# Kernel optimization log

Hardware: AMD Instinct MI355X
Metric: run time of the kernel (lower is better)

Reference implementation:

```python
import jax, jax.numpy as jnp
import numpy as np

D_MODEL = 2048
N_HEADS = 16
HEAD_DIM = D_MODEL // N_HEADS


def setup_inputs() -> dict:
    key = jax.random.key(0)
    k_x, k_wqkv, k_bqkv, k_wo, k_bo = jax.random.split(key, 5)
    s = 1.0 / np.sqrt(D_MODEL)
    return {
        "x": jax.random.normal(k_x, (2, 2048, D_MODEL), dtype=jnp.float32),
        "w_qkv": jax.random.uniform(k_wqkv, (D_MODEL, 3 * D_MODEL), jnp.float32, -s, s),
        "b_qkv": jax.random.uniform(k_bqkv, (3 * D_MODEL,), jnp.float32, -s, s),
        "w_out": jax.random.uniform(k_wo, (D_MODEL, D_MODEL), jnp.float32, -s, s),
        "b_out": jax.random.uniform(k_bo, (D_MODEL,), jnp.float32, -s, s),
    }


def reference(x, w_qkv, b_qkv, w_out, b_out):
    b, l, d = x.shape
    h, e = N_HEADS, HEAD_DIM
    qkv = x @ w_qkv + b_qkv                       # [b, l, 3d]
    q, k, v = jnp.split(qkv, 3, axis=-1)
    # split heads: [b, l, d] -> [b, l, h, e]
    q = q.reshape(b, l, h, e)
    k = k.reshape(b, l, h, e)
    v = v.reshape(b, l, h, e)
    scale = 1.0 / np.sqrt(e).astype(np.float32)
    scores = jnp.einsum("bqhe,bkhe->bhqk", q, k) * scale  # [b, h, l, l]
    attn = jax.nn.softmax(scores, axis=-1)                 # non-causal (module hardcodes is_causal=False)
    out = jnp.einsum("bhqk,bkhe->bqhe", attn, v)           # [b, l, h, e]
    out = out.reshape(b, l, d)                             # merge heads
    return out @ w_out + b_out
```

## Files before the change

### kernel.cpp

```cpp
#include <hip/hip_runtime.h>

typedef __attribute__((ext_vector_type(8))) short bf16x8;
typedef __attribute__((ext_vector_type(4))) float f32x4;
typedef __attribute__((ext_vector_type(16))) float f32x16;
typedef __attribute__((ext_vector_type(4))) int int4v;
typedef __attribute__((ext_vector_type(4))) unsigned short us4;

#define LOG2E 1.4426950408889634f

__device__ __forceinline__ unsigned short f2b(float f){
  unsigned u = __builtin_bit_cast(unsigned, f);
  u = (u + 0x7fffu + ((u >> 16) & 1u)) >> 16;
  return (unsigned short)u;
}
__device__ __forceinline__ unsigned short f2bf(float f){
  unsigned u = __builtin_bit_cast(unsigned, f);
  return (unsigned short)((u + 0x8000u) >> 16);
}

__device__ __forceinline__ f32x4 mfma16(bf16x8 a, bf16x8 b, f32x4 c){
  return __builtin_amdgcn_mfma_f32_16x16x32_bf16(a, b, c, 0, 0, 0);
}
__device__ __forceinline__ f32x16 mfma32(bf16x8 a, bf16x8 b, f32x16 c){
  return __builtin_amdgcn_mfma_f32_32x32x16_bf16(a, b, c, 0, 0, 0);
}

typedef const __attribute__((address_space(1))) void* gas_t;
typedef __attribute__((address_space(3))) void* las_t;
__device__ __forceinline__ void glds16(const void* g, void* l){
  __builtin_amdgcn_global_load_lds((gas_t)g, (las_t)l, 16, 0, 0);
}

__global__ __launch_bounds__(256) void cast_bf16_kernel(const float4* __restrict__ in,
                                                        us4* __restrict__ out, int n4){
  int i = blockIdx.x * 256 + threadIdx.x;
  int stride = gridDim.x * 256;
  for (; i < n4; i += stride){
    float4 v = in[i];
    us4 o; o.x = f2b(v.x); o.y = f2b(v.y); o.z = f2b(v.z); o.w = f2b(v.w);
    out[i] = o;
  }
}

__global__ __launch_bounds__(256) void transpose_cast_kernel(const float* __restrict__ in,
                                                             unsigned short* __restrict__ out,
                                                             int R, int C){
  __shared__ float tile[64][65];
  const int tid = threadIdx.x;
  const int c0 = blockIdx.x * 64, r0 = blockIdx.y * 64;
#pragma unroll
  for (int p = 0; p < 4; p++){
    int idx = p * 1024 + tid * 4;
    int rr = idx >> 6, cc = idx & 63;
    float4 v = *(const float4*)(in + (size_t)(r0 + rr) * C + (c0 + cc));
    tile[rr][cc+0] = v.x; tile[rr][cc+1] = v.y; tile[rr][cc+2] = v.z; tile[rr][cc+3] = v.w;
  }
  __syncthreads();
#pragma unroll
  for (int p = 0; p < 4; p++){
    int idx = p * 1024 + tid * 4;
    int crow = idx >> 6, rcol = idx & 63;
    us4 o;
    o.x = f2b(tile[rcol+0][crow]); o.y = f2b(tile[rcol+1][crow]);
    o.z = f2b(tile[rcol+2][crow]); o.w = f2b(tile[rcol+3][crow]);
    *(us4*)(out + (size_t)(c0 + crow) * R + (r0 + rcol)) = o;
  }
}

template<int MODE>
__global__ __launch_bounds__(256, 2) void gemm_kernel(
    const unsigned short* __restrict__ A,
    const unsigned short* __restrict__ BT,
    const float* __restrict__ bias,
    unsigned short* __restrict__ qb,
    unsigned short* __restrict__ kb,
    unsigned short* __restrict__ vtb,
    float* __restrict__ outp)
{
  constexpr int K = 2048;
  constexpr int NT = K / 64;
  __shared__ short lA[2][128 * 64];
  __shared__ short lB[2][128 * 64];
  const int tid = threadIdx.x, lane = tid & 63, wid = tid >> 6;
  const int l16 = lane & 15, lhi = lane >> 4;
  const int wr = wid >> 1, wc = wid & 1;
  const int bm = blockIdx.x, bn = blockIdx.y;

  const char* Abase = (const char*)(A + (size_t)bm * 128 * K);
  const char* Bbase = (const char*)(BT + (size_t)bn * 128 * K);

  const char* agp[4]; const char* bgp[4];
  int dst[4];
#pragma unroll
  for (int i = 0; i < 4; i++){
    int c = wid * 4 + i;
    int row = c * 8 + (lane >> 3);
    int col = ((lane & 7) * 16) ^ ((lane >> 3) << 4);
    agp[i] = Abase + (size_t)row * (K * 2) + col;
    bgp[i] = Bbase + (size_t)row * (K * 2) + col;
    dst[i] = c * 1024;
  }

  auto stage = [&](int kt, int buf){
    char* bA = (char*)lA[buf]; char* bB = (char*)lB[buf];
#pragma unroll
    for (int i = 0; i < 4; i++){
      glds16(agp[i] + kt * 128, bA + dst[i]);
      glds16(bgp[i] + kt * 128, bB + dst[i]);
    }
  };

  f32x4 acc[4][4];
  f32x4 z = {0.f, 0.f, 0.f, 0.f};
#pragma unroll
  for (int i = 0; i < 4; i++)
#pragma unroll
    for (int j = 0; j < 4; j++) acc[i][j] = z;

  stage(0, 0);
  __syncthreads();
  int cur = 0;
  for (int kt = 0; kt < NT; ++kt){
    if (kt + 1 < NT) stage(kt + 1, cur ^ 1);
#pragma unroll
    for (int kk = 0; kk < 2; kk++){
      bf16x8 af[4], bfr[4];
#pragma unroll
      for (int mf = 0; mf < 4; mf++){
        int row = wr * 64 + mf * 16 + l16;
        int byte = (row * 128 + kk * 64 + lhi * 16) ^ ((row & 7) << 4);
        af[mf] = *(const bf16x8*)((const char*)lA[cur] + byte);
      }
#pragma unroll
      for (int nf = 0; nf < 4; nf++){
        int row = wc * 64 + nf * 16 + l16;
        int byte = (row * 128 + kk * 64 + lhi * 16) ^ ((row & 7) << 4);
        bfr[nf] = *(const bf16x8*)((const char*)lB[cur] + byte);
      }
      __builtin_amdgcn_s_setprio(1);
#pragma unroll
      for (int mf = 0; mf < 4; mf++)
#pragma unroll
        for (int nf = 0; nf < 4; nf++)
          acc[mf][nf] = mfma16(af[mf], bfr[nf], acc[mf][nf]);
      __builtin_amdgcn_s_setprio(0);
    }
    __syncthreads();
    cur ^= 1;
  }

  const int row0 = bm * 128 + wr * 64;
  const int col0 = bn * 128 + wc * 64;
  if (MODE == 0){
#pragma unroll
    for (int nf = 0; nf < 4; nf++){
      int colb = col0 + nf * 16;
      float bv = bias[colb + l16];
      int which = colb >> 11;
      int h = (colb >> 7) & 15;
      int e = (colb & 127) + l16;
#pragma unroll
      for (int mf = 0; mf < 4; mf++){
#pragma unroll
        for (int r = 0; r < 4; r++){
          int row = row0 + mf * 16 + lhi * 4 + r;
          int b = row >> 11, t = row & 2047;
          float v = acc[mf][nf][r] + bv;
          size_t bh = (size_t)(b * 16 + h);
          if (which == 0)      qb[(bh * 2048 + t) * 128 + e] = f2b(v * 0.08838834764831845f);
          else if (which == 1) kb[(bh * 2048 + t) * 128 + e] = f2b(v);
          else                 vtb[(bh * 128 + e) * 2048 + t] = f2b(v);
        }
      }
    }
  } else {
#pragma unroll
    for (int nf = 0; nf < 4; nf++){
      int col = col0 + nf * 16 + l16;
      float bv = bias[col];
#pragma unroll
      for (int mf = 0; mf < 4; mf++){
#pragma unroll
        for (int r = 0; r < 4; r++){
          int row = row0 + mf * 16 + lhi * 4 + r;
          outp[(size_t)row * 2048 + col] = acc[mf][nf][r] + bv;
        }
      }
    }
  }
}

__global__ __launch_bounds__(256, 2) void attn_kernel(
    const unsigned short* __restrict__ q_buf,
    const unsigned short* __restrict__ k_buf,
    const unsigned short* __restrict__ vt_buf,
    unsigned short* __restrict__ attn_out)
{
  constexpr int L = 2048, NT = L / 64;
  __shared__ short lK[2][64 * 128];
  __shared__ short lVT[2][128 * 64];
  const int tid = threadIdx.x, lane = tid & 63, wid = tid >> 6;
  const int l31 = lane & 31, lhi2 = lane >> 5;

  const int d = blockIdx.y * 16 + blockIdx.x;
  const int bh = (d & 7) + 8 * ((d >> 3) & 3);
  const int qi = d >> 5;
  const int qbase = qi * 128;

  const unsigned short* qp = q_buf + (size_t)bh * L * 128;
  const char* kp2 = (const char*)(k_buf + (size_t)bh * L * 128);
  const char* vp2 = (const char*)(vt_buf + (size_t)bh * 128 * L);

  bf16x8 qf[8];
  {
    const unsigned short* qr = qp + (size_t)(qbase + wid * 32 + l31) * 128 + lhi2 * 8;
#pragma unroll
    for (int kk = 0; kk < 8; kk++)
      qf[kk] = *(const bf16x8*)(qr + kk * 16);
  }

  const char* kgp[4]; const char* vgp[4];
  int kdst[4], vdst[4];
#pragma unroll
  for (int i = 0; i < 4; i++){
    int c = wid * 4 + i;
    { int row = c * 4 + (lane >> 4);
      int col = ((lane & 15) * 16) ^ ((row & 7) << 4);
      kgp[i] = kp2 + row * 256 + col;
      kdst[i] = c * 1024; }
    { int e = c * 8 + (lane >> 3);
      int col = ((lane & 7) * 16) ^ ((e & 7) << 4);
      vgp[i] = vp2 + (size_t)e * 4096 + col;
      vdst[i] = c * 1024; }
  }

  auto stage = [&](int kt, int buf){
    char* bK = (char*)lK[buf]; char* bV = (char*)lVT[buf];
#pragma unroll
    for (int i = 0; i < 4; i++){
      glds16(kgp[i] + kt * 16384, bK + kdst[i]);
      glds16(vgp[i] + (size_t)kt * 128, bV + vdst[i]);
    }
  };

  f32x16 oacc[4];
#pragma unroll
  for (int nf = 0; nf < 4; nf++)
#pragma unroll
    for (int j = 0; j < 16; j++) oacc[nf][j] = 0.f;
  float m = -1e30f, ml2 = 0.f, lsum = 0.f;

  stage(0, 0);
  __syncthreads();
  int cur = 0;
  for (int kt = 0; kt < NT; ++kt){
    if (kt + 1 < NT) stage(kt + 1, cur ^ 1);
    const char* cK = (const char*)lK[cur];
    const char* cV = (const char*)lVT[cur];

    f32x16 sf[2];
#pragma unroll
    for (int mf = 0; mf < 2; mf++)
#pragma unroll
      for (int j = 0; j < 16; j++) sf[mf][j] = 0.f;
    __builtin_amdgcn_s_setprio(1);
#pragma unroll
    for (int kk = 0; kk < 8; kk++){
#pragma unroll
      for (int mf = 0; mf < 2; mf++){
        int byte = ((l31 * 256 + kk * 32 + lhi2 * 16) ^ ((l31 & 7) << 4)) + mf * 8192;
        bf16x8 kf = *(const bf16x8*)(cK + byte);
        sf[mf] = mfma32(kf, qf[kk], sf[mf]);
      }
    }
    __builtin_amdgcn_s_setprio(0);

    float tm = sf[0][0];
#pragma unroll
    for (int mf = 0; mf < 2; mf++)
#pragma unroll
      for (int j = 0; j < 16; j++) tm = fmaxf(tm, sf[mf][j]);
    tm = fmaxf(tm, __shfl_xor(tm, 32, 64));

    if (!__all(tm <= m + 8.0f)){
      float mn = fmaxf(m, tm);
      float alpha = __builtin_exp2f((m - mn) * LOG2E);
      m = mn; ml2 = mn * LOG2E;
      lsum *= alpha;
#pragma unroll
      for (int reg = 0; reg < 16; reg++){
        int row = (reg & 3) + 8 * (reg >> 2) + 4 * lhi2;
        float ar = __shfl(alpha, row | (lane & 32), 64);
#pragma unroll
        for (int nf = 0; nf < 4; nf++) oacc[nf][reg] *= ar;
      }
    }

    float pex[2][16];
    float rs = 0.f;
#pragma unroll
    for (int mf = 0; mf < 2; mf++)
#pragma unroll
      for (int j = 0; j < 16; j++){
        float p = __builtin_exp2f(__builtin_fmaf(sf[mf][j], LOG2E, -ml2));
        pex[mf][j] = p; rs += p;
      }
    rs += __shfl_xor(rs, 32, 64);
    lsum += rs;

    unsigned W[2][4][2];
#pragma unroll
    for (int mf = 0; mf < 2; mf++)
#pragma unroll
      for (int g = 0; g < 4; g++)
#pragma unroll
        for (int h = 0; h < 2; h++)
          W[mf][g][h] = (unsigned)f2bf(pex[mf][g * 4 + 2 * h]) |
                        ((unsigned)f2bf(pex[mf][g * 4 + 2 * h + 1]) << 16);

    __builtin_amdgcn_s_setprio(1);
#pragma unroll
    for (int kk2 = 0; kk2 < 4; kk2++){
      const int mfp = kk2 >> 1, gA = 2 * (kk2 & 1), gB = gA + 1;
      unsigned A0 = W[mfp][gA][0], A1 = W[mfp][gA][1];
      unsigned B0 = W[mfp][gB][0], B1 = W[mfp][gB][1];
      unsigned own0 = lhi2 ? B0 : A0, own1 = lhi2 ? B1 : A1;
      unsigned snd0 = lhi2 ? A0 : B0, snd1 = lhi2 ? A1 : B1;
      unsigned rcv0 = (unsigned)__shfl_xor((int)snd0, 32, 64);
      unsigned rcv1 = (unsigned)__shfl_xor((int)snd1, 32, 64);
      int4v pw;
      pw.x = (int)(lhi2 ? rcv0 : own0);
      pw.y = (int)(lhi2 ? rcv1 : own1);
      pw.z = (int)(lhi2 ? own0 : rcv0);
      pw.w = (int)(lhi2 ? own1 : rcv1);
      bf16x8 pa = __builtin_bit_cast(bf16x8, pw);
#pragma unroll
      for (int nf = 0; nf < 4; nf++){
        int byte = ((l31 * 128 + kk2 * 32 + lhi2 * 16) ^ ((l31 & 7) << 4)) + nf * 4096;
        bf16x8 vb = *(const bf16x8*)(cV + byte);
        oacc[nf] = mfma32(pa, vb, oacc[nf]);
      }
    }
    __builtin_amdgcn_s_setprio(0);

    __syncthreads();
    cur ^= 1;
  }

  const int b = bh >> 4, h = bh & 15;
  float rl = 1.0f / lsum;
#pragma unroll
  for (int reg = 0; reg < 16; reg++){
    int row = (reg & 3) + 8 * (reg >> 2) + 4 * lhi2;
    float rr = __shfl(rl, row | (lane & 32), 64);
    size_t base = ((size_t)(b * L + qbase + wid * 32 + row)) * 2048 + h * 128 + l31;
#pragma unroll
    for (int nf = 0; nf < 4; nf++)
      attn_out[base + nf * 32] = f2b(oacc[nf][reg] * rr);
  }
}

extern "C" void kernel_launch(void* const* d_in, const int* in_sizes, int n_in,
                              void* d_out, int out_size, void* d_ws, size_t ws_size,
                              hipStream_t stream) {
  const float* x     = (const float*)d_in[0];
  const float* w_qkv = (const float*)d_in[1];
  const float* b_qkv = (const float*)d_in[2];
  const float* w_out = (const float*)d_in[3];
  const float* b_out = (const float*)d_in[4];
  float* out = (float*)d_out;

  unsigned short* ws = (unsigned short*)d_ws;
  unsigned short* xb    = ws;
  unsigned short* wqkvT = xb    + (size_t)4096 * 2048;
  unsigned short* woutT = wqkvT + (size_t)6144 * 2048;
  unsigned short* qb    = woutT + (size_t)2048 * 2048;
  unsigned short* kb    = qb    + (size_t)2 * 16 * 2048 * 128;
  unsigned short* vtb   = kb    + (size_t)2 * 16 * 2048 * 128;
  unsigned short* attnb = vtb   + (size_t)2 * 16 * 2048 * 128;

  cast_bf16_kernel<<<2048, 256, 0, stream>>>((const float4*)x, (us4*)xb, (4096 * 2048) / 4);
  transpose_cast_kernel<<<dim3(96, 32), 256, 0, stream>>>(w_qkv, wqkvT, 2048, 6144);
  transpose_cast_kernel<<<dim3(32, 32), 256, 0, stream>>>(w_out, woutT, 2048, 2048);
  gemm_kernel<0><<<dim3(32, 48), 256, 0, stream>>>(xb, wqkvT, b_qkv, qb, kb, vtb, nullptr);
  attn_kernel<<<dim3(16, 32), 256, 0, stream>>>(qb, kb, vtb, attnb);
  gemm_kernel<1><<<dim3(32, 16), 256, 0, stream>>>(attnb, woutT, b_out, nullptr, nullptr, nullptr, out);
}
```

Before: 280.0 us.

## Widen GEMM tiles to 128x256 with 512 threads and explicit vmcnt pipelining

The GEMM kernel now uses 512-thread blocks, eight waves each owning a 64x64 output tile, so every block covers a 128x256 output tile. The B tile buffer doubles in size, and the grid halves along N for both the QKV and output projections. The main loop now issues the next two stages ahead, uses explicit s_waitcnt vmcnt plus raw s_barrier instead of __syncthreads, and refills a buffer right after its last read. This is meant to raise A-tile reuse and overlap global loads with MFMA work, at the cost of more LDS per block, one block per CU, and fewer blocks for the output GEMM (256).

```diff
diff --git a/kernel.cpp b/kernel.cpp
--- a/kernel.cpp
+++ b/kernel.cpp
@@ -68,7 +68,7 @@
 }
 
 template<int MODE>
-__global__ __launch_bounds__(256, 2) void gemm_kernel(
+__global__ __launch_bounds__(512, 1) void gemm_kernel(
     const unsigned short* __restrict__ A,
     const unsigned short* __restrict__ BT,
     const float* __restrict__ bias,
@@ -80,34 +80,37 @@
   constexpr int K = 2048;
   constexpr int NT = K / 64;
   __shared__ short lA[2][128 * 64];
-  __shared__ short lB[2][128 * 64];
+  __shared__ short lB[2][256 * 64];
   const int tid = threadIdx.x, lane = tid & 63, wid = tid >> 6;
   const int l16 = lane & 15, lhi = lane >> 4;
-  const int wr = wid >> 1, wc = wid & 1;
+  const int wm = wid >> 2, wn = wid & 3;
   const int bm = blockIdx.x, bn = blockIdx.y;
 
   const char* Abase = (const char*)(A + (size_t)bm * 128 * K);
-  const char* Bbase = (const char*)(BT + (size_t)bn * 128 * K);
-
-  const char* agp[4]; const char* bgp[4];
-  int dst[4];
-#pragma unroll
-  for (int i = 0; i < 4; i++){
-    int c = wid * 4 + i;
-    int row = c * 8 + (lane >> 3);
-    int col = ((lane & 7) * 16) ^ ((lane >> 3) << 4);
-    agp[i] = Abase + (size_t)row * (K * 2) + col;
-    bgp[i] = Bbase + (size_t)row * (K * 2) + col;
-    dst[i] = c * 1024;
+  const char* Bbase = (const char*)(BT + (size_t)bn * 256 * K);
+
+  const int scol = ((lane & 7) * 16) ^ ((lane >> 3) << 4);
+  const char* agp[2]; const char* bgp[4];
+  int adst[2], bdst[4];
+#pragma unroll
+  for (int j = 0; j < 2; j++){
+    int row = j * 64 + wid * 8 + (lane >> 3);
+    agp[j] = Abase + (size_t)row * (K * 2) + scol;
+    adst[j] = (j * 64 + wid * 8) * 128;
+  }
+#pragma unroll
+  for (int j = 0; j < 4; j++){
+    int row = j * 64 + wid * 8 + (lane >> 3);
+    bgp[j] = Bbase + (size_t)row * (K * 2) + scol;
+    bdst[j] = (j * 64 + wid * 8) * 128;
   }
 
   auto stage = [&](int kt, int buf){
     char* bA = (char*)lA[buf]; char* bB = (char*)lB[buf];
 #pragma unroll
-    for (int i = 0; i < 4; i++){
-      glds16(agp[i] + kt * 128, bA + dst[i]);
-      glds16(bgp[i] + kt * 128, bB + dst[i]);
-    }
+    for (int j = 0; j < 2; j++) glds16(agp[j] + kt * 128, bA + adst[j]);
+#pragma unroll
+    for (int j = 0; j < 4; j++) glds16(bgp[j] + kt * 128, bB + bdst[j]);
   };
 
   f32x4 acc[4][4];
@@ -117,25 +120,30 @@
 #pragma unroll
     for (int j = 0; j < 4; j++) acc[i][j] = z;
 
-  stage(0, 0);
-  __syncthreads();
-  int cur = 0;
-  for (int kt = 0; kt < NT; ++kt){
-    if (kt + 1 < NT) stage(kt + 1, cur ^ 1);
+  stage(0, 0); stage(1, 1);
+
+  for (int t = 0; t < NT; ++t){
+    const int c = t & 1;
+    if (t < NT - 1) asm volatile("s_waitcnt vmcnt(6)" ::: "memory");
+    else            asm volatile("s_waitcnt vmcnt(0)" ::: "memory");
+    __builtin_amdgcn_sched_barrier(0);
+    __builtin_amdgcn_s_barrier();
+    __builtin_amdgcn_sched_barrier(0);
+
 #pragma unroll
     for (int kk = 0; kk < 2; kk++){
       bf16x8 af[4], bfr[4];
 #pragma unroll
       for (int mf = 0; mf < 4; mf++){
-        int row = wr * 64 + mf * 16 + l16;
+        int row = wm * 64 + mf * 16 + l16;
         int byte = (row * 128 + kk * 64 + lhi * 16) ^ ((row & 7) << 4);
-        af[mf] = *(const bf16x8*)((const char*)lA[cur] + byte);
+        af[mf] = *(const bf16x8*)((const char*)lA[c] + byte);
       }
 #pragma unroll
       for (int nf = 0; nf < 4; nf++){
-        int row = wc * 64 + nf * 16 + l16;
+        int row = wn * 64 + nf * 16 + l16;
         int byte = (row * 128 + kk * 64 + lhi * 16) ^ ((row & 7) << 4);
-        bfr[nf] = *(const bf16x8*)((const char*)lB[cur] + byte);
+        bfr[nf] = *(const bf16x8*)((const char*)lB[c] + byte);
       }
       __builtin_amdgcn_s_setprio(1);
 #pragma unroll
@@ -145,12 +153,16 @@
           acc[mf][nf] = mfma16(af[mf], bfr[nf], acc[mf][nf]);
       __builtin_amdgcn_s_setprio(0);
     }
-    __syncthreads();
-    cur ^= 1;
-  }
-
-  const int row0 = bm * 128 + wr * 64;
-  const int col0 = bn * 128 + wc * 64;
+
+    asm volatile("s_waitcnt lgkmcnt(0)" ::: "memory");
+    __builtin_amdgcn_sched_barrier(0);
+    __builtin_amdgcn_s_barrier();
+    __builtin_amdgcn_sched_barrier(0);
+    if (t + 2 < NT) stage(t + 2, c);
+  }
+
+  const int row0 = bm * 128 + wm * 64;
+  const int col0 = bn * 256 + wn * 64;
   if (MODE == 0){
 #pragma unroll
     for (int nf = 0; nf < 4; nf++){
@@ -382,7 +394,7 @@
   cast_bf16_kernel<<<2048, 256, 0, stream>>>((const float4*)x, (us4*)xb, (4096 * 2048) / 4);
   transpose_cast_kernel<<<dim3(96, 32), 256, 0, stream>>>(w_qkv, wqkvT, 2048, 6144);
   transpose_cast_kernel<<<dim3(32, 32), 256, 0, stream>>>(w_out, woutT, 2048, 2048);
-  gemm_kernel<0><<<dim3(32, 48), 256, 0, stream>>>(xb, wqkvT, b_qkv, qb, kb, vtb, nullptr);
+  gemm_kernel<0><<<dim3(32, 24), 512, 0, stream>>>(xb, wqkvT, b_qkv, qb, kb, vtb, nullptr);
   attn_kernel<<<dim3(16, 32), 256, 0, stream>>>(qb, kb, vtb, attnb);
-  gemm_kernel<1><<<dim3(32, 16), 256, 0, stream>>>(attnb, woutT, b_out, nullptr, nullptr, nullptr, out);
-}
+  gemm_kernel<1><<<dim3(32, 8), 512, 0, stream>>>(attnb, woutT, b_out, nullptr, nullptr, nullptr, out);
+}
```

After: 306.0 us. 9.3% more time.

## Use 256x256 eight-wave GEMM with quadrant-phased pipelining for QKV projection

Applied to the files above, without the earlier changes.

Replaces the QKV projection GEMM with a new 512-thread kernel that computes 256x256 output tiles. Each K step is split into four quadrant phases that interleave LDS fragment reads, async global-to-LDS staging of the next tile half, barriers and MFMA bursts at raised priority. Both GEMMs now launch as 1D grids remapped so that groups of blocks sharing the same A rows run together, to improve L2 reuse. The larger tile raises arithmetic intensity but uses 128KB of LDS and allows one block per CU. It also depends on precise vmcnt bookkeeping, which is fragile.

```diff
diff --git a/kernel.cpp b/kernel.cpp
--- a/kernel.cpp
+++ b/kernel.cpp
@@ -30,6 +30,10 @@
 __device__ __forceinline__ void glds16(const void* g, void* l){
   __builtin_amdgcn_global_load_lds((gas_t)g, (las_t)l, 16, 0, 0);
 }
+
+#define VMW(N) asm volatile("s_waitcnt vmcnt(" #N ")" ::: "memory")
+#define BARX() do{ __builtin_amdgcn_sched_barrier(0); __builtin_amdgcn_s_barrier(); \
+                   __builtin_amdgcn_sched_barrier(0); }while(0)
 
 __global__ __launch_bounds__(256) void cast_bf16_kernel(const float4* __restrict__ in,
                                                         us4* __restrict__ out, int n4){
@@ -64,6 +68,121 @@
     o.x = f2b(tile[rcol+0][crow]); o.y = f2b(tile[rcol+1][crow]);
     o.z = f2b(tile[rcol+2][crow]); o.w = f2b(tile[rcol+3][crow]);
     *(us4*)(out + (size_t)(c0 + crow) * R + (r0 + rcol)) = o;
+  }
+}
+
+__global__ __launch_bounds__(512, 1) void gemm8_kernel(
+    const unsigned short* __restrict__ A,
+    const unsigned short* __restrict__ BT,
+    const float* __restrict__ bias,
+    unsigned short* __restrict__ qb,
+    unsigned short* __restrict__ kb,
+    unsigned short* __restrict__ vtb)
+{
+  constexpr int K = 2048;
+  constexpr int NT = K / 64;
+  __shared__ short lds[2][4][128 * 64];
+  const int tid = threadIdx.x, lane = tid & 63, wid = tid >> 6;
+  const int l16 = lane & 15, lhi = lane >> 4;
+  const int wm = wid >> 2, wn = wid & 3;
+
+  const int id = blockIdx.x;
+  const int logical = (id & 7) * 48 + (id >> 3);
+  const int bm = logical & 15, bn = logical >> 4;
+
+  const char* Ab = (const char*)(A + (size_t)bm * 256 * K);
+  const char* Bb = (const char*)(BT + (size_t)bn * 256 * K);
+
+  const int scol = ((lane & 7) * 16) ^ ((lane >> 3) << 4);
+  const char* gsrc[4][2];
+  int gdst[2];
+#pragma unroll
+  for (int j = 0; j < 2; j++){
+    int r = j * 64 + wid * 8 + (lane >> 3);
+    gdst[j] = (j * 64 + wid * 8) * 128;
+    gsrc[0][j] = Ab + (size_t)(r      ) * (K * 2) + scol;
+    gsrc[1][j] = Ab + (size_t)(r + 128) * (K * 2) + scol;
+    gsrc[2][j] = Bb + (size_t)(r      ) * (K * 2) + scol;
+    gsrc[3][j] = Bb + (size_t)(r + 128) * (K * 2) + scol;
+  }
+  auto stageH = [&](int kt, int buf, int h){
+    char* dstb = (char*)lds[buf][h];
+#pragma unroll
+    for (int j = 0; j < 2; j++) glds16(gsrc[h][j] + (size_t)kt * 128, dstb + gdst[j]);
+  };
+
+  f32x4 acc[8][4];
+  f32x4 z = {0.f, 0.f, 0.f, 0.f};
+#pragma unroll
+  for (int i = 0; i < 8; i++)
+#pragma unroll
+    for (int j = 0; j < 4; j++) acc[i][j] = z;
+
+#define PHASE(MQ, NQ, SH)                                                        \
+  {                                                                              \
+    bf16x8 af[4][2], bfr[2][2];                                                  \
+    const char* aH = (const char*)lds[cur][MQ];                                  \
+    const char* bH = (const char*)lds[cur][2 + NQ];                              \
+    _Pragma("unroll")                                                            \
+    for (int mf2 = 0; mf2 < 4; mf2++){                                           \
+      int r = wm * 64 + mf2 * 16 + l16;                                          \
+      _Pragma("unroll")                                                          \
+      for (int kk = 0; kk < 2; kk++)                                             \
+        af[mf2][kk] = *(const bf16x8*)(aH + ((r * 128 + kk * 64 + lhi * 16) ^ ((r & 7) << 4))); \
+    }                                                                            \
+    _Pragma("unroll")                                                            \
+    for (int nf2 = 0; nf2 < 2; nf2++){                                           \
+      int r = wn * 32 + nf2 * 16 + l16;                                          \
+      _Pragma("unroll")                                                          \
+      for (int kk = 0; kk < 2; kk++)                                             \
+        bfr[nf2][kk] = *(const bf16x8*)(bH + ((r * 128 + kk * 64 + lhi * 16) ^ ((r & 7) << 4))); \
+    }                                                                            \
+    if (st) stageH(t + 1, cur ^ 1, SH);                                          \
+    BARX();                                                                      \
+    __builtin_amdgcn_s_setprio(1);                                               \
+    _Pragma("unroll")                                                            \
+    for (int kk = 0; kk < 2; kk++)                                               \
+      _Pragma("unroll")                                                          \
+      for (int mf2 = 0; mf2 < 4; mf2++)                                          \
+        _Pragma("unroll")                                                        \
+        for (int nf2 = 0; nf2 < 2; nf2++)                                        \
+          acc[MQ*4+mf2][NQ*2+nf2] = mfma16(af[mf2][kk], bfr[nf2][kk], acc[MQ*4+mf2][NQ*2+nf2]); \
+    __builtin_amdgcn_s_setprio(0);                                               \
+  }
+
+  stageH(0, 0, 0); stageH(0, 0, 2); stageH(0, 0, 3); stageH(0, 0, 1);
+  VMW(4);
+  BARX();
+
+  for (int t = 0; t < NT; ++t){
+    const int cur = t & 1;
+    const bool st = (t + 1 < NT);
+    PHASE(0, 0, 0);  if (st) { VMW(4); } else { VMW(2); }  BARX();
+    PHASE(0, 1, 2);  if (st) { VMW(4); } else { VMW(0); }  BARX();
+    PHASE(1, 0, 3);                                        BARX();
+    PHASE(1, 1, 1);  if (st) { VMW(4); }                   BARX();
+  }
+#undef PHASE
+
+  const int row00 = bm * 256, col00 = bn * 256;
+#pragma unroll
+  for (int nf = 0; nf < 4; nf++){
+    int gcol = col00 + (nf >> 1) * 128 + wn * 32 + (nf & 1) * 16 + l16;
+    float bv = bias[gcol];
+    int which = gcol >> 11, h = (gcol >> 7) & 15, e = gcol & 127;
+#pragma unroll
+    for (int mf = 0; mf < 8; mf++){
+#pragma unroll
+      for (int r = 0; r < 4; r++){
+        int grow = row00 + (mf >> 2) * 128 + wm * 64 + (mf & 3) * 16 + lhi * 4 + r;
+        int b = grow >> 11, tt = grow & 2047;
+        float v = acc[mf][nf][r] + bv;
+        size_t bh = (size_t)(b * 16 + h);
+        if (which == 0)      qb[(bh * 2048 + tt) * 128 + e] = f2b(v * 0.08838834764831845f);
+        else if (which == 1) kb[(bh * 2048 + tt) * 128 + e] = f2b(v);
+        else                 vtb[(bh * 128 + e) * 2048 + tt] = f2b(v);
+      }
+    }
   }
 }
 
@@ -84,7 +203,10 @@
   const int tid = threadIdx.x, lane = tid & 63, wid = tid >> 6;
   const int l16 = lane & 15, lhi = lane >> 4;
   const int wr = wid >> 1, wc = wid & 1;
-  const int bm = blockIdx.x, bn = blockIdx.y;
+
+  const int id = blockIdx.x;
+  const int logical = (id & 7) * 64 + (id >> 3);
+  const int bm = logical & 31, bn = logical >> 5;
 
   const char* Abase = (const char*)(A + (size_t)bm * 128 * K);
   const char* Bbase = (const char*)(BT + (size_t)bn * 128 * K);
@@ -382,7 +504,7 @@
   cast_bf16_kernel<<<2048, 256, 0, stream>>>((const float4*)x, (us4*)xb, (4096 * 2048) / 4);
   transpose_cast_kernel<<<dim3(96, 32), 256, 0, stream>>>(w_qkv, wqkvT, 2048, 6144);
   transpose_cast_kernel<<<dim3(32, 32), 256, 0, stream>>>(w_out, woutT, 2048, 2048);
-  gemm_kernel<0><<<dim3(32, 48), 256, 0, stream>>>(xb, wqkvT, b_qkv, qb, kb, vtb, nullptr);
+  gemm8_kernel<<<384, 512, 0, stream>>>(xb, wqkvT, b_qkv, qb, kb, vtb);
   attn_kernel<<<dim3(16, 32), 256, 0, stream>>>(qb, kb, vtb, attnb);
-  gemm_kernel<1><<<dim3(32, 16), 256, 0, stream>>>(attnb, woutT, b_out, nullptr, nullptr, nullptr, out);
-}
+  gemm_kernel<1><<<512, 256, 0, stream>>>(attnb, woutT, b_out, nullptr, nullptr, nullptr, out);
+}
```

New measurement: 332.4 us. 1.19x slower.

## Deepen GEMM pipeline to four LDS stages with explicit vmcnt waits

Applied to the files above, without the earlier changes.

The GEMM kernel now uses 32-wide K tiles in a four-buffer ring, with three tiles of global-to-LDS prefetch in flight. It replaces the double-buffered 64-wide tiles and syncthreads with explicit vmcnt waits and raw barriers, and adjusts the LDS swizzle for the new 64-byte rows. The aim is to hide global load latency better in both projection GEMMs. In exchange it runs twice as many loop iterations, each with two barriers and less MFMA work, which adds barrier overhead.

```diff
diff --git a/kernel.cpp b/kernel.cpp
--- a/kernel.cpp
+++ b/kernel.cpp
@@ -30,6 +30,10 @@
 __device__ __forceinline__ void glds16(const void* g, void* l){
   __builtin_amdgcn_global_load_lds((gas_t)g, (las_t)l, 16, 0, 0);
 }
+
+#define VMW(N) asm volatile("s_waitcnt vmcnt(" #N ")" ::: "memory")
+#define SBAR() do{ __builtin_amdgcn_sched_barrier(0); __builtin_amdgcn_s_barrier(); \
+                   __builtin_amdgcn_sched_barrier(0); }while(0)
 
 __global__ __launch_bounds__(256) void cast_bf16_kernel(const float4* __restrict__ in,
                                                         us4* __restrict__ out, int n4){
@@ -68,7 +72,7 @@
 }
 
 template<int MODE>
-__global__ __launch_bounds__(256, 2) void gemm_kernel(
+__global__ __launch_bounds__(256, 2) void gemm4_kernel(
     const unsigned short* __restrict__ A,
     const unsigned short* __restrict__ BT,
     const float* __restrict__ bias,
@@ -78,9 +82,9 @@
     float* __restrict__ outp)
 {
   constexpr int K = 2048;
-  constexpr int NT = K / 64;
-  __shared__ short lA[2][128 * 64];
-  __shared__ short lB[2][128 * 64];
+  constexpr int NT = K / 32;
+  __shared__ short lA[4][128 * 32];
+  __shared__ short lB[4][128 * 32];
   const int tid = threadIdx.x, lane = tid & 63, wid = tid >> 6;
   const int l16 = lane & 15, lhi = lane >> 4;
   const int wr = wid >> 1, wc = wid & 1;
@@ -89,25 +93,23 @@
   const char* Abase = (const char*)(A + (size_t)bm * 128 * K);
   const char* Bbase = (const char*)(BT + (size_t)bn * 128 * K);
 
-  const char* agp[4]; const char* bgp[4];
-  int dst[4];
-#pragma unroll
-  for (int i = 0; i < 4; i++){
-    int c = wid * 4 + i;
-    int row = c * 8 + (lane >> 3);
-    int col = ((lane & 7) * 16) ^ ((lane >> 3) << 4);
-    agp[i] = Abase + (size_t)row * (K * 2) + col;
-    bgp[i] = Bbase + (size_t)row * (K * 2) + col;
-    dst[i] = c * 1024;
-  }
-
-  auto stage = [&](int kt, int buf){
+  const char* agp[2]; const char* bgp[2];
+  int dst2[2];
+#pragma unroll
+  for (int j = 0; j < 2; j++){
+    int r = j * 64 + wid * 16 + (lane >> 2);
+    int colb = ((lane & 3) << 4) ^ (((r >> 1) & 3) << 4);
+    agp[j] = Abase + (size_t)r * (K * 2) + colb;
+    bgp[j] = Bbase + (size_t)r * (K * 2) + colb;
+    dst2[j] = j * 4096 + wid * 1024;
+  }
+
+  auto stage = [&](int t, int buf){
     char* bA = (char*)lA[buf]; char* bB = (char*)lB[buf];
-#pragma unroll
-    for (int i = 0; i < 4; i++){
-      glds16(agp[i] + kt * 128, bA + dst[i]);
-      glds16(bgp[i] + kt * 128, bB + dst[i]);
-    }
+    glds16(agp[0] + t * 64, bA + dst2[0]);
+    glds16(agp[1] + t * 64, bA + dst2[1]);
+    glds16(bgp[0] + t * 64, bB + dst2[0]);
+    glds16(bgp[1] + t * 64, bB + dst2[1]);
   };
 
   f32x4 acc[4][4];
@@ -117,36 +119,40 @@
 #pragma unroll
     for (int j = 0; j < 4; j++) acc[i][j] = z;
 
-  stage(0, 0);
-  __syncthreads();
-  int cur = 0;
-  for (int kt = 0; kt < NT; ++kt){
-    if (kt + 1 < NT) stage(kt + 1, cur ^ 1);
-#pragma unroll
-    for (int kk = 0; kk < 2; kk++){
-      bf16x8 af[4], bfr[4];
-#pragma unroll
-      for (int mf = 0; mf < 4; mf++){
-        int row = wr * 64 + mf * 16 + l16;
-        int byte = (row * 128 + kk * 64 + lhi * 16) ^ ((row & 7) << 4);
-        af[mf] = *(const bf16x8*)((const char*)lA[cur] + byte);
-      }
-#pragma unroll
-      for (int nf = 0; nf < 4; nf++){
-        int row = wc * 64 + nf * 16 + l16;
-        int byte = (row * 128 + kk * 64 + lhi * 16) ^ ((row & 7) << 4);
-        bfr[nf] = *(const bf16x8*)((const char*)lB[cur] + byte);
-      }
-      __builtin_amdgcn_s_setprio(1);
-#pragma unroll
-      for (int mf = 0; mf < 4; mf++)
-#pragma unroll
-        for (int nf = 0; nf < 4; nf++)
-          acc[mf][nf] = mfma16(af[mf], bfr[nf], acc[mf][nf]);
-      __builtin_amdgcn_s_setprio(0);
-    }
-    __syncthreads();
-    cur ^= 1;
+  stage(0, 0); stage(1, 1); stage(2, 2);
+
+  for (int t = 0; t < NT; ++t){
+    if (t < NT - 2)      { VMW(8); }
+    else if (t == NT - 2){ VMW(4); }
+    else                 { VMW(0); }
+    SBAR();
+    if (t + 3 < NT) stage(t + 3, (t + 3) & 3);
+
+    const char* cA = (const char*)lA[t & 3];
+    const char* cB = (const char*)lB[t & 3];
+    bf16x8 af[4], bfr[4];
+#pragma unroll
+    for (int mf = 0; mf < 4; mf++){
+      int row = wr * 64 + mf * 16 + l16;
+      int byte = (row * 64 + lhi * 16) ^ (((row >> 1) & 3) << 4);
+      af[mf] = *(const bf16x8*)(cA + byte);
+    }
+#pragma unroll
+    for (int nf = 0; nf < 4; nf++){
+      int row = wc * 64 + nf * 16 + l16;
+      int byte = (row * 64 + lhi * 16) ^ (((row >> 1) & 3) << 4);
+      bfr[nf] = *(const bf16x8*)(cB + byte);
+    }
+    __builtin_amdgcn_s_setprio(1);
+#pragma unroll
+    for (int mf = 0; mf < 4; mf++)
+#pragma unroll
+      for (int nf = 0; nf < 4; nf++)
+        acc[mf][nf] = mfma16(af[mf], bfr[nf], acc[mf][nf]);
+    __builtin_amdgcn_s_setprio(0);
+
+    asm volatile("s_waitcnt lgkmcnt(0)" ::: "memory");
+    SBAR();
   }
 
   const int row0 = bm * 128 + wr * 64;
@@ -164,12 +170,12 @@
 #pragma unroll
         for (int r = 0; r < 4; r++){
           int row = row0 + mf * 16 + lhi * 4 + r;
-          int b = row >> 11, t = row & 2047;
+          int b = row >> 11, tt = row & 2047;
           float v = acc[mf][nf][r] + bv;
           size_t bh = (size_t)(b * 16 + h);
-          if (which == 0)      qb[(bh * 2048 + t) * 128 + e] = f2b(v * 0.08838834764831845f);
-          else if (which == 1) kb[(bh * 2048 + t) * 128 + e] = f2b(v);
-          else                 vtb[(bh * 128 + e) * 2048 + t] = f2b(v);
+          if (which == 0)      qb[(bh * 2048 + tt) * 128 + e] = f2b(v * 0.08838834764831845f);
+          else if (which == 1) kb[(bh * 2048 + tt) * 128 + e] = f2b(v);
+          else                 vtb[(bh * 128 + e) * 2048 + tt] = f2b(v);
         }
       }
     }
@@ -382,7 +388,7 @@
   cast_bf16_kernel<<<2048, 256, 0, stream>>>((const float4*)x, (us4*)xb, (4096 * 2048) / 4);
   transpose_cast_kernel<<<dim3(96, 32), 256, 0, stream>>>(w_qkv, wqkvT, 2048, 6144);
   transpose_cast_kernel<<<dim3(32, 32), 256, 0, stream>>>(w_out, woutT, 2048, 2048);
-  gemm_kernel<0><<<dim3(32, 48), 256, 0, stream>>>(xb, wqkvT, b_qkv, qb, kb, vtb, nullptr);
+  gemm4_kernel<0><<<dim3(32, 48), 256, 0, stream>>>(xb, wqkvT, b_qkv, qb, kb, vtb, nullptr);
   attn_kernel<<<dim3(16, 32), 256, 0, stream>>>(qb, kb, vtb, attnb);
-  gemm_kernel<1><<<dim3(32, 16), 256, 0, stream>>>(attnb, woutT, b_out, nullptr, nullptr, nullptr, out);
-}
+  gemm4_kernel<1><<<dim3(32, 16), 256, 0, stream>>>(attnb, woutT, b_out, nullptr, nullptr, nullptr, out);
+}
```

New measurement: 317.1 us. 13.3% more time.
